# Optimization experiments

Hardware: AMD Instinct MI355X
Metric: run time of the kernel (lower is better)

The kernel has to match this reference:

```python
import jax, jax.numpy as jnp
import numpy as np

# module config (matches init_kwargs, single stream, groups=1)
N, I = 4, 64            # batch, input channels
CR, CA, CO = 64, 64, 64 # recurrent, attention, out channels
HEADS, S = 4, 3         # heads, spatial kernel
HC = CA // HEADS        # head channels = 16
H, W = 48, 48
INIT_I, INIT_F = -1.0, 1.0


def _conv(x, w, padding):
    # x: [N,C,H,W], w: [O,C,kh,kw]
    return jax.lax.conv_general_dilated(
        x, w, window_strides=(1, 1), padding=padding,
        dimension_numbers=('NCHW', 'OIHW', 'NCHW'))


def setup_inputs() -> dict:
    key = jax.random.key(0)
    ks = jax.random.split(key, 8)
    std = 0.05
    x = jax.random.normal(ks[0], (N, I, H, W), jnp.float32)
    W_in = jax.random.normal(ks[1], (CR, I), jnp.float32) * std      # 1x1 input conv
    b_in = jnp.zeros((CR,), jnp.float32)
    # 4 combos (xx, xh, hx, hh), each a 3x3 conv CR->CA, no bias
    Wq = jax.random.normal(ks[2], (4, CA, CR, S, S), jnp.float32) * std * (HC ** -0.5)
    Wk = jax.random.normal(ks[3], (4, CA, CR, S, S), jnp.float32) * std
    Wv = jax.random.normal(ks[4], (4, CA, CR, S, S), jnp.float32) * std
    # gate projections: 4 gates (i,f,g,o) x 4 attn branches, each 1x1 CA->CR
    Wproj = jax.random.normal(ks[5], (4, 4, CR, CA), jnp.float32) * std * 0.5
    b_gates = jnp.array([INIT_I, INIT_F, 0.0, 0.0], jnp.float32)[:, None] * jnp.ones((4, CR), jnp.float32)
    W_out = jax.random.normal(ks[6], (CO, CR), jnp.float32) * std    # 1x1 out conv
    b_out = jnp.zeros((CO,), jnp.float32)
    return {"x": x, "W_in": W_in, "b_in": b_in, "Wq": Wq, "Wk": Wk, "Wv": Wv,
            "Wproj": Wproj, "b_gates": b_gates, "W_out": W_out, "b_out": b_out}


def reference(x, W_in, b_in, Wq, Wk, Wv, Wproj, b_gates, W_out, b_out):
    n, _, hh, ww = x.shape
    # input projection (Accumulate of one 1x1 conv, bias 0)
    xin = jnp.einsum('nchw,oc->nohw', x, W_in) + b_in[None, :, None, None]
    h = jnp.zeros_like(xin)  # cold start: past is empty -> h = c = 0
    pairs = ((xin, xin), (xin, h), (h, xin), (h, h))
    attns = []
    for idx, (query, token) in enumerate(pairs):
        # q: SAME-padded 3x3 conv -> Q = H*W tokens; k/v: VALID -> D = (H-2)*(W-2)
        q = _conv(query, Wq[idx], 'SAME').reshape(n, HEADS, HC, -1)    # [n,h,c,Q]
        k = _conv(token, Wk[idx], 'VALID').reshape(n, HEADS, HC, -1)   # [n,h,c,D]
        v = _conv(token, Wv[idx], 'VALID').reshape(n, HEADS, HC, -1)   # [n,h,c,D]
        w = jax.nn.softmax(jnp.einsum('nhcq,nhcd->nhqd', q, k), axis=-1)
        a = jnp.einsum('nhcd,nhqd->nhcq', v, w).reshape(n, CA, hh, ww)
        attns.append(a)
    A = jnp.stack(attns, axis=0)  # [4, n, CA, H, W]
    # Accumulate of 4 1x1 projections per gate + gate bias
    pre = jnp.einsum('anchw,gaoc->gnohw', A, Wproj) + b_gates[:, None, :, None, None]
    i = jax.nn.sigmoid(pre[0])
    f = jax.nn.sigmoid(pre[1])
    g = jnp.tanh(pre[2])
    o = jax.nn.sigmoid(pre[3])
    c = i * g          # c_prev = 0, so f*c_prev vanishes
    hout = o * jnp.tanh(c)  # dropout p=0 -> identity
    return jnp.einsum('nchw,oc->nohw', hout, W_out) + b_out[None, :, None, None]
```

## Files before the change

### kernel.cpp

```cpp
#include <hip/hip_runtime.h>
#include <math.h>

#define NB   4
#define CIN  64
#define HH   48
#define WW   48
#define HW   2304
#define DH   46
#define DW   46
#define DD   2116
#define NHEAD 4
#define HC   16
#define NT   136
#define QTL  144
#define GS   20000

typedef short  s4 __attribute__((ext_vector_type(4)));
typedef short  s8 __attribute__((ext_vector_type(8)));
typedef float  f4 __attribute__((ext_vector_type(4)));

__device__ __forceinline__ void split4(f4 a, s4& hi, s4& lo) {
    #pragma unroll
    for (int r = 0; r < 4; ++r) {
        unsigned u = __builtin_bit_cast(unsigned, a[r]);
        hi[r] = (short)(u >> 16);
        float l = a[r] - __builtin_bit_cast(float, u & 0xffff0000u);
        lo[r] = (short)(__builtin_bit_cast(unsigned, l) >> 16);
    }
}

__global__ __launch_bounds__(256) void k_xw(const float* __restrict__ x,
                                            const float* __restrict__ Win,
                                            const float* __restrict__ bin,
                                            const float* __restrict__ Wq,
                                            const float* __restrict__ Wk,
                                            const float* __restrict__ Wv,
                                            unsigned short* __restrict__ xb,
                                            unsigned short* __restrict__ Wb,
                                            float* __restrict__ a2m) {
    int b = blockIdx.x;
    if (b == 784) {
        a2m[threadIdx.x] = 0.f;
        return;
    }
    if (b < 640) {
        int bx = b % 10, n = (b / 10) & 3, ocg = b / 40;
        int cell = bx * 256 + threadIdx.x;
        if (cell >= 2500) return;
        int cy = cell / 50, cx = cell - cy * 50;
        float a[4] = {0.f, 0.f, 0.f, 0.f};
        if (cy >= 1 && cy <= 48 && cx >= 1 && cx <= 48) {
            int px = (cy - 1) * 48 + (cx - 1);
            const float* xp = x + (size_t)(n * CIN) * HW + px;
            #pragma unroll
            for (int j = 0; j < 4; ++j) a[j] = bin[ocg * 4 + j];
            #pragma unroll 8
            for (int ic = 0; ic < CIN; ++ic) {
                float xv = xp[ic * HW];
                a[0] += Win[(ocg * 4 + 0) * CIN + ic] * xv;
                a[1] += Win[(ocg * 4 + 1) * CIN + ic] * xv;
                a[2] += Win[(ocg * 4 + 2) * CIN + ic] * xv;
                a[3] += Win[(ocg * 4 + 3) * CIN + ic] * xv;
            }
        }
        s8 st;
        #pragma unroll
        for (int j = 0; j < 4; ++j) {
            unsigned u = __builtin_bit_cast(unsigned, a[j]);
            st[j] = (short)(u >> 16);
            float lo = a[j] - __builtin_bit_cast(float, u & 0xffff0000u);
            st[4 + j] = (short)(__builtin_bit_cast(unsigned, lo) >> 16);
        }
        *(s8*)(xb + ((size_t)(n * 16 + ocg) * 2500 + cell) * 8) = st;
    } else {
        int bx = b - 640;
        int cq = bx / 9, tap = bx - cq * 9;
        int cv = cq >> 2, ocq = cq & 3;
        const float* src = (cv == 0) ? Wq : (cv == 1) ? Wk : (cv == 2) ? Wv
                                                          : (Wv + 2 * CIN * CIN * 9);
        int t = threadIdx.x;
        int m = t >> 4, kl = t & 15, quad = kl >> 2, j = kl & 3;
        #pragma unroll
        for (int kq = 0; kq < 4; ++kq) {
            float v = src[((size_t)(ocq * 16 + m) * CIN + kq * 16 + kl) * 9 + tap];
            unsigned u = __builtin_bit_cast(unsigned, v);
            float lo = v - __builtin_bit_cast(float, u & 0xffff0000u);
            size_t base = ((size_t)(cq * 9 + tap) * 4 + kq) * 512 + m * 32 + quad * 8 + j;
            Wb[base]     = (unsigned short)(u >> 16);
            Wb[base + 4] = (unsigned short)(__builtin_bit_cast(unsigned, lo) >> 16);
        }
    }
}

__global__ __launch_bounds__(256, 3) void k_conv(const unsigned short* __restrict__ xb,
                                                 const unsigned short* __restrict__ Wb,
                                                 unsigned short* __restrict__ Qb,
                                                 float* __restrict__ k0,
                                                 float* __restrict__ v0,
                                                 float* __restrict__ a2m) {
    int y = blockIdx.x, n = blockIdx.y, cv = blockIdx.z;
    int outw = (cv == 0) ? 48 : 46;
    int pd   = (cv == 0) ? 0 : 1;
    if (y >= outw) return;
    int lane = threadIdx.x & 63, wv = threadIdx.x >> 6;
    int m16 = lane & 15, quad = lane >> 4;
    const unsigned short* Wt = Wb + (size_t)(cv * 4 + wv) * 9 * 2048 + m16 * 32 + quad * 8;
    const unsigned short* B0 = xb + (size_t)(n * 16 + quad) * GS
                                  + ((size_t)(y + pd) * 50 + pd + m16) * 8;

    f4 a0 = {0.f, 0.f, 0.f, 0.f}, a1 = a0, a2 = a0;

    s8 w[4], c0[4], c1[4], c2[4];
    #pragma unroll
    for (int kq = 0; kq < 4; ++kq) {
        w[kq]  = *(const s8*)(Wt + kq * 512);
        c0[kq] = *(const s8*)(B0 + (size_t)kq * 4 * GS);
        c1[kq] = *(const s8*)(B0 + (size_t)kq * 4 * GS + 128);
        c2[kq] = *(const s8*)(B0 + (size_t)kq * 4 * GS + 256);
    }
    __builtin_amdgcn_sched_group_barrier(0x020, 16, 0);

    #pragma unroll
    for (int tap = 0; tap < 9; ++tap) {
        s8 wn[4], n0[4], n1[4], n2[4];
        if (tap < 8) {
            int tn = tap + 1;
            int dy = tn / 3, dx = tn - dy * 3;
            const unsigned short* bq = B0 + (size_t)(dy * 50 + dx) * 8;
            const unsigned short* wp = Wt + tn * 2048;
            #pragma unroll
            for (int kq = 0; kq < 4; ++kq) {
                wn[kq] = *(const s8*)(wp + kq * 512);
                n0[kq] = *(const s8*)(bq + (size_t)kq * 4 * GS);
                n1[kq] = *(const s8*)(bq + (size_t)kq * 4 * GS + 128);
                n2[kq] = *(const s8*)(bq + (size_t)kq * 4 * GS + 256);
            }
        }
        #pragma unroll
        for (int kq = 0; kq < 4; ++kq) {
            s4 ah  = __builtin_shufflevector(w[kq], w[kq], 0, 1, 2, 3);
            s4 al  = __builtin_shufflevector(w[kq], w[kq], 4, 5, 6, 7);
            s4 bh0 = __builtin_shufflevector(c0[kq], c0[kq], 0, 1, 2, 3);
            s4 bl0 = __builtin_shufflevector(c0[kq], c0[kq], 4, 5, 6, 7);
            s4 bh1 = __builtin_shufflevector(c1[kq], c1[kq], 0, 1, 2, 3);
            s4 bl1 = __builtin_shufflevector(c1[kq], c1[kq], 4, 5, 6, 7);
            s4 bh2 = __builtin_shufflevector(c2[kq], c2[kq], 0, 1, 2, 3);
            s4 bl2 = __builtin_shufflevector(c2[kq], c2[kq], 4, 5, 6, 7);
            a0 = __builtin_amdgcn_mfma_f32_16x16x16bf16_1k(ah, bh0, a0, 0, 0, 0);
            a1 = __builtin_amdgcn_mfma_f32_16x16x16bf16_1k(ah, bh1, a1, 0, 0, 0);
            a2 = __builtin_amdgcn_mfma_f32_16x16x16bf16_1k(ah, bh2, a2, 0, 0, 0);
            a0 = __builtin_amdgcn_mfma_f32_16x16x16bf16_1k(al, bh0, a0, 0, 0, 0);
            a1 = __builtin_amdgcn_mfma_f32_16x16x16bf16_1k(al, bh1, a1, 0, 0, 0);
            a2 = __builtin_amdgcn_mfma_f32_16x16x16bf16_1k(al, bh2, a2, 0, 0, 0);
            a0 = __builtin_amdgcn_mfma_f32_16x16x16bf16_1k(ah, bl0, a0, 0, 0, 0);
            a1 = __builtin_amdgcn_mfma_f32_16x16x16bf16_1k(ah, bl1, a1, 0, 0, 0);
            a2 = __builtin_amdgcn_mfma_f32_16x16x16bf16_1k(ah, bl2, a2, 0, 0, 0);
        }
        if (tap < 8) __builtin_amdgcn_sched_group_barrier(0x020, 16, 0);
        __builtin_amdgcn_sched_group_barrier(0x008, 36, 0);
        if (tap < 8) {
            #pragma unroll
            for (int kq = 0; kq < 4; ++kq) {
                w[kq] = wn[kq]; c0[kq] = n0[kq]; c1[kq] = n1[kq]; c2[kq] = n2[kq];
            }
        }
    }

    if (cv == 0) {
        int nh = n * 4 + wv;
        unsigned short* dst = Qb + ((size_t)(nh * QTL + y * 3)) * 512 + m16 * 16 + quad * 4;
        f4 accs[3] = {a0, a1, a2};
        #pragma unroll
        for (int xt = 0; xt < 3; ++xt) {
            s4 hi, lo;
            split4(accs[xt], hi, lo);
            *(s4*)(dst + xt * 512) = hi;
            *(s4*)(dst + xt * 512 + 256) = lo;
        }
    } else if (cv == 3) {
        #pragma unroll
        for (int r = 0; r < 4; ++r) {
            float t = a0[r] + a1[r] + ((m16 < 14) ? a2[r] : 0.f);
            t += __shfl_xor(t, 1); t += __shfl_xor(t, 2);
            t += __shfl_xor(t, 4); t += __shfl_xor(t, 8);
            if (m16 == 0)
                atomicAdd(&a2m[n * CIN + wv * 16 + quad * 4 + r], t);
        }
    } else {
        float* ob = (cv == 1) ? k0 : v0;
        size_t outsz = (size_t)DD;
        float* opb = ob + (size_t)(n * CIN + wv * 16 + quad * 4) * outsz + (size_t)y * DW;
        {
            float* op = opb + m16;
            op[0] = a0.x; op[outsz] = a0.y; op[2 * outsz] = a0.z; op[3 * outsz] = a0.w;
            op = opb + 16 + m16;
            op[0] = a1.x; op[outsz] = a1.y; op[2 * outsz] = a1.z; op[3 * outsz] = a1.w;
        }
        if (32 + m16 < DW) {
            float* op = opb + 32 + m16;
            op[0] = a2.x; op[outsz] = a2.y; op[2 * outsz] = a2.z; op[3 * outsz] = a2.w;
        }
    }
}

__global__ __launch_bounds__(256) void k_cvt(const float* __restrict__ k0,
                                             const float* __restrict__ v0,
                                             unsigned short* __restrict__ Kb,
                                             unsigned short* __restrict__ Vb) {
    __shared__ float sm[272];
    int bx = blockIdx.x, nh = blockIdx.y;
    int n = nh >> 2, h = nh & 3;
    int t = threadIdx.x;
    int c = t >> 4, d = t & 15;
    int dgl = bx * 16 + d;
    float kv = (dgl < DD) ? k0[(size_t)(n * CIN + h * HC + c) * DD + dgl] : 0.f;
    sm[c * 17 + d] = kv;
    __syncthreads();
    {
        int d2 = t >> 4, c2 = t & 15;
        float v = sm[c2 * 17 + d2];
        unsigned u = __builtin_bit_cast(unsigned, v);
        unsigned short* dst = Kb + (size_t)(nh * NT + bx) * 512;
        dst[t] = (unsigned short)(u >> 16);
        float lo = v - __builtin_bit_cast(float, u & 0xffff0000u);
        dst[256 + t] = (unsigned short)(__builtin_bit_cast(unsigned, lo) >> 16);
    }
    {
        float vv = (dgl < DD) ? v0[(size_t)(n * CIN + h * HC + c) * DD + dgl] : 0.f;
        unsigned u = __builtin_bit_cast(unsigned, vv);
        unsigned short* dst = Vb + (size_t)(nh * NT + bx) * 512;
        dst[t] = (unsigned short)(u >> 16);
        float lo = vv - __builtin_bit_cast(float, u & 0xffff0000u);
        dst[256 + t] = (unsigned short)(__builtin_bit_cast(unsigned, lo) >> 16);
    }
}

__global__ __launch_bounds__(256) void k_mattn(const unsigned short* __restrict__ Qb,
                                               const unsigned short* __restrict__ Kb,
                                               const unsigned short* __restrict__ Vb,
                                               float* __restrict__ part) {
    __shared__ float sO[4][4][256];
    __shared__ float sl[4][4][64];
    int strip = blockIdx.x >> 1, hb = blockIdx.x & 1, nh = blockIdx.y;
    int lane = threadIdx.x & 63, wv = threadIdx.x >> 6;
    int ds = hb * 4 + wv;
    int q16 = lane & 15, quad = lane >> 4;
    int foff = q16 * 16 + quad * 4;

    s4 qh[4], ql[4];
    #pragma unroll
    for (int j = 0; j < 4; ++j) {
        const unsigned short* Qp = Qb + (size_t)(nh * QTL + strip * 4 + j) * 512 + foff;
        qh[j] = *(const s4*)(Qp);
        ql[j] = *(const s4*)(Qp + 256);
    }
    f4 O[4];
    float l[4];
    #pragma unroll
    for (int j = 0; j < 4; ++j) { O[j] = (f4){0.f, 0.f, 0.f, 0.f}; l[j] = 0.f; }

    const unsigned short* Kp = Kb + (size_t)(nh * NT + ds * 17) * 512 + foff;
    const unsigned short* Vp = Vb + (size_t)(nh * NT + ds * 17) * 512 + foff;
    s4 khi = *(const s4*)(Kp);
    s4 klo = *(const s4*)(Kp + 256);
    s4 vhi = *(const s4*)(Vp);
    s4 vlo = *(const s4*)(Vp + 256);

    for (int it = 0; it < 17; ++it) {
        int nxt = (it < 16) ? (it + 1) * 512 : 0;
        s4 nkhi = *(const s4*)(Kp + nxt);
        s4 nklo = *(const s4*)(Kp + nxt + 256);
        s4 nvhi = *(const s4*)(Vp + nxt);
        s4 nvlo = *(const s4*)(Vp + nxt + 256);

        #pragma unroll
        for (int j = 0; j < 4; ++j) {
            f4 c1 = (f4){0.f, 0.f, 0.f, 0.f};
            c1 = __builtin_amdgcn_mfma_f32_16x16x16bf16_1k(khi, qh[j], c1, 0, 0, 0);
            c1 = __builtin_amdgcn_mfma_f32_16x16x16bf16_1k(klo, qh[j], c1, 0, 0, 0);
            c1 = __builtin_amdgcn_mfma_f32_16x16x16bf16_1k(khi, ql[j], c1, 0, 0, 0);
            float p0 = __expf(c1.x), p1 = __expf(c1.y);
            float p2 = __expf(c1.z), p3 = __expf(c1.w);
            l[j] += (p0 + p1) + (p2 + p3);
            unsigned u0 = __builtin_bit_cast(unsigned, p0);
            unsigned u1 = __builtin_bit_cast(unsigned, p1);
            unsigned u2 = __builtin_bit_cast(unsigned, p2);
            unsigned u3 = __builtin_bit_cast(unsigned, p3);
            s4 ph;
            ph.x = (short)(u0 >> 16); ph.y = (short)(u1 >> 16);
            ph.z = (short)(u2 >> 16); ph.w = (short)(u3 >> 16);
            float r0 = p0 - __builtin_bit_cast(float, u0 & 0xffff0000u);
            float r1 = p1 - __builtin_bit_cast(float, u1 & 0xffff0000u);
            float r2 = p2 - __builtin_bit_cast(float, u2 & 0xffff0000u);
            float r3 = p3 - __builtin_bit_cast(float, u3 & 0xffff0000u);
            s4 pl;
            pl.x = (short)(__builtin_bit_cast(unsigned, r0) >> 16);
            pl.y = (short)(__builtin_bit_cast(unsigned, r1) >> 16);
            pl.z = (short)(__builtin_bit_cast(unsigned, r2) >> 16);
            pl.w = (short)(__builtin_bit_cast(unsigned, r3) >> 16);
            O[j] = __builtin_amdgcn_mfma_f32_16x16x16bf16_1k(vhi, ph, O[j], 0, 0, 0);
            O[j] = __builtin_amdgcn_mfma_f32_16x16x16bf16_1k(vlo, ph, O[j], 0, 0, 0);
            O[j] = __builtin_amdgcn_mfma_f32_16x16x16bf16_1k(vhi, pl, O[j], 0, 0, 0);
        }
        khi = nkhi; klo = nklo; vhi = nvhi; vlo = nvlo;
    }

    #pragma unroll
    for (int j = 0; j < 4; ++j) {
        sO[wv][j][(quad * 4 + 0) * 16 + q16] = O[j].x;
        sO[wv][j][(quad * 4 + 1) * 16 + q16] = O[j].y;
        sO[wv][j][(quad * 4 + 2) * 16 + q16] = O[j].z;
        sO[wv][j][(quad * 4 + 3) * 16 + q16] = O[j].w;
        sl[wv][j][quad * 16 + q16] = l[j];
    }
    __syncthreads();
    int t = threadIdx.x;
    float* pb = part + (size_t)((nh * 36 + strip) * 2 + hb) * 1280;
    #pragma unroll
    for (int j = 0; j < 4; ++j)
        pb[j * 256 + t] = (sO[0][j][t] + sO[1][j][t]) + (sO[2][j][t] + sO[3][j][t]);
    {
        int j2 = t >> 6, i2 = t & 63;
        pb[1024 + t] = (sl[0][j2][i2] + sl[1][j2][i2]) + (sl[2][j2][i2] + sl[3][j2][i2]);
    }
}

__global__ __launch_bounds__(256) void k_gates(const float* __restrict__ part,
                                               const float* __restrict__ a2m,
                                               const float* __restrict__ Wproj,
                                               const float* __restrict__ bg,
                                               const float* __restrict__ Wout,
                                               const float* __restrict__ bout,
                                               float* __restrict__ out) {
    __shared__ float a0s[64][16];
    __shared__ float wps[3][64][64];
    __shared__ float hs[16][68];
    __shared__ float invs[4][16];
    __shared__ float c2s[3][64];
    int n = blockIdx.y;
    int pt = blockIdx.x;
    int strip = pt >> 2, jq = pt & 3;
    int p0 = pt * 16;
    int tid = threadIdx.x;

    if (tid < 64) {
        int h = tid >> 4, q = tid & 15;
        const float* b0 = part + (size_t)(((n * 4 + h) * 36 + strip) * 2) * 1280;
        const float* b1 = b0 + 1280;
        float s = 0.f;
        #pragma unroll
        for (int quad = 0; quad < 4; ++quad)
            s += b0[1024 + jq * 64 + quad * 16 + q] + b1[1024 + jq * 64 + quad * 16 + q];
        invs[h][q] = 1.f / (s - 60.f);
    } else {
        int gi = (tid - 64) >> 6, o = tid & 63;
        int g = (gi == 0) ? 0 : (gi == 1) ? 2 : 3;
        float acc = bg[g * CIN + o];
        const float* wp = Wproj + ((size_t)(g * 4 + 2) * CIN + o) * CIN;
        const float* am = a2m + n * CIN;
        #pragma unroll 8
        for (int c = 0; c < CIN; ++c) acc += wp[c] * (am[c] * (1.f / 2116.f));
        c2s[gi][o] = acc;
    }
    __syncthreads();

    for (int idx = tid; idx < 1024; idx += 256) {
        int c = idx >> 4, px = idx & 15;
        int h = c >> 4, c16 = c & 15;
        const float* b0 = part + (size_t)(((n * 4 + h) * 36 + strip) * 2) * 1280;
        const float* b1 = b0 + 1280;
        int off = jq * 256 + c16 * 16 + px;
        a0s[c][px] = (b0[off] + b1[off]) * invs[h][px];
    }
    for (int idx = tid; idx < 12288; idx += 256) {
        int o = idx & 63; int rest = idx >> 6; int c = rest & 63; int gi = rest >> 6;
        int g = (gi == 0) ? 0 : (gi == 1) ? 2 : 3;
        wps[gi][c][o] = Wproj[((size_t)(g * 4 + 0) * CIN + o) * CIN + c];
    }
    __syncthreads();

    int o = tid & 63, pg = tid >> 6;
    float pi[4], pgt[4], po[4];
    {
        float ci = c2s[0][o], cg = c2s[1][o], co = c2s[2][o];
        #pragma unroll
        for (int j = 0; j < 4; ++j) { pi[j] = ci; pgt[j] = cg; po[j] = co; }
    }
    const float4* a4 = (const float4*)&a0s[0][0];
    #pragma unroll 4
    for (int c = 0; c < 64; ++c) {
        float4 av = a4[c * 4 + pg];
        float w0 = wps[0][c][o], w1 = wps[1][c][o], w2 = wps[2][c][o];
        pi[0]  += w0 * av.x; pi[1]  += w0 * av.y; pi[2]  += w0 * av.z; pi[3]  += w0 * av.w;
        pgt[0] += w1 * av.x; pgt[1] += w1 * av.y; pgt[2] += w1 * av.z; pgt[3] += w1 * av.w;
        po[0]  += w2 * av.x; po[1]  += w2 * av.y; po[2]  += w2 * av.z; po[3]  += w2 * av.w;
    }
    #pragma unroll
    for (int j = 0; j < 4; ++j) {
        float ii = 1.f / (1.f + __expf(-pi[j]));
        float gg = tanhf(pgt[j]);
        float oo = 1.f / (1.f + __expf(-po[j]));
        float cc = ii * gg;
        hs[pg * 4 + j][o] = oo * tanhf(cc);
    }
    __syncthreads();
    float acc[4];
    float bo = bout[o];
    #pragma unroll
    for (int j = 0; j < 4; ++j) acc[j] = bo;
    const float* wo = Wout + o * CIN;
    #pragma unroll 2
    for (int cg_ = 0; cg_ < 16; ++cg_) {
        float w0 = wo[cg_ * 4 + 0], w1 = wo[cg_ * 4 + 1], w2 = wo[cg_ * 4 + 2], w3 = wo[cg_ * 4 + 3];
        #pragma unroll
        for (int j = 0; j < 4; ++j) {
            const float4 hv = *(const float4*)&hs[pg * 4 + j][cg_ * 4];
            acc[j] += w0 * hv.x + w1 * hv.y + w2 * hv.z + w3 * hv.w;
        }
    }
    #pragma unroll
    for (int j = 0; j < 4; ++j)
        out[(size_t)(n * CIN + o) * HW + p0 + pg * 4 + j] = acc[j];
}

extern "C" void kernel_launch(void* const* d_in, const int* in_sizes, int n_in,
                              void* d_out, int out_size, void* d_ws, size_t ws_size,
                              hipStream_t stream) {
    const float* x     = (const float*)d_in[0];
    const float* W_in  = (const float*)d_in[1];
    const float* b_in  = (const float*)d_in[2];
    const float* Wq    = (const float*)d_in[3];
    const float* Wk    = (const float*)d_in[4];
    const float* Wv    = (const float*)d_in[5];
    const float* Wproj = (const float*)d_in[6];
    const float* b_g   = (const float*)d_in[7];
    const float* W_out = (const float*)d_in[8];
    const float* b_out = (const float*)d_in[9];
    float* out = (float*)d_out;

    float* k0   = (float*)d_ws;
    float* v0   = k0 + 541696;
    float* a2m  = v0 + 541696;
    float* part = a2m + 256;
    unsigned short* Qb = (unsigned short*)(part + 1474560);
    unsigned short* Kb = Qb + (size_t)16 * QTL * 512;
    unsigned short* Vb = Kb + (size_t)16 * NT * 512;
    unsigned short* xb = Vb + (size_t)16 * NT * 512;
    unsigned short* Wb = xb + (size_t)4 * 16 * 2500 * 8;

    k_xw    <<<dim3(785), 256, 0, stream>>>(x, W_in, b_in, Wq, Wk, Wv, xb, Wb, a2m);
    k_conv  <<<dim3(48, 4, 4), 256, 0, stream>>>(xb, Wb, Qb, k0, v0, a2m);
    k_cvt   <<<dim3(136, 16), 256, 0, stream>>>(k0, v0, Kb, Vb);
    k_mattn <<<dim3(72, 16), 256, 0, stream>>>(Qb, Kb, Vb, part);
    k_gates <<<dim3(144, 4), 256, 0, stream>>>(part, a2m, Wproj, b_g, W_out, b_out, out);
}
```

Baseline: 176.4 us.

## Use 16x16x32 bf16 MFMA, write K/V directly from conv, drop convert kernel

```diff
diff --git a/kernel.cpp b/kernel.cpp
--- a/kernel.cpp
+++ b/kernel.cpp
@@ -6,18 +6,22 @@
 #define HH   48
 #define WW   48
 #define HW   2304
-#define DH   46
-#define DW   46
 #define DD   2116
 #define NHEAD 4
 #define HC   16
-#define NT   136
+#define NT   144
 #define QTL  144
-#define GS   20000
+#define PS   40000
 
 typedef short  s4 __attribute__((ext_vector_type(4)));
 typedef short  s8 __attribute__((ext_vector_type(8)));
 typedef float  f4 __attribute__((ext_vector_type(4)));
+typedef __bf16 b8 __attribute__((ext_vector_type(8)));
+
+__device__ __forceinline__ f4 mm32(s8 a, s8 b, f4 c) {
+    return __builtin_amdgcn_mfma_f32_16x16x32_bf16(
+        __builtin_bit_cast(b8, a), __builtin_bit_cast(b8, b), c, 0, 0, 0);
+}
 
 __device__ __forceinline__ void split4(f4 a, s4& hi, s4& lo) {
     #pragma unroll
@@ -37,10 +41,21 @@
                                             const float* __restrict__ Wv,
                                             unsigned short* __restrict__ xb,
                                             unsigned short* __restrict__ Wb,
-                                            float* __restrict__ a2m) {
+                                            float* __restrict__ a2m,
+                                            unsigned short* __restrict__ Kb,
+                                            unsigned short* __restrict__ Vb) {
     int b = blockIdx.x;
     if (b == 784) {
         a2m[threadIdx.x] = 0.f;
+        return;
+    }
+    if (b > 784) {
+        int nh = b - 785;
+        s8 z = (s8){0, 0, 0, 0, 0, 0, 0, 0};
+        for (int i = threadIdx.x; i < 1152; i += 256) {
+            if (i < 384) *(s8*)(Kb + ((size_t)nh * NT + 138) * 512  + (size_t)i * 8) = z;
+            else         *(s8*)(Vb + ((size_t)nh * NT + 138) * 1024 + (size_t)(i - 384) * 8) = z;
+        }
         return;
     }
     if (b < 640) {
@@ -63,15 +78,18 @@
                 a[3] += Win[(ocg * 4 + 3) * CIN + ic] * xv;
             }
         }
-        s8 st;
+        s4 hi, lo;
         #pragma unroll
         for (int j = 0; j < 4; ++j) {
             unsigned u = __builtin_bit_cast(unsigned, a[j]);
-            st[j] = (short)(u >> 16);
-            float lo = a[j] - __builtin_bit_cast(float, u & 0xffff0000u);
-            st[4 + j] = (short)(__builtin_bit_cast(unsigned, lo) >> 16);
-        }
-        *(s8*)(xb + ((size_t)(n * 16 + ocg) * 2500 + cell) * 8) = st;
+            hi[j] = (short)(u >> 16);
+            float l = a[j] - __builtin_bit_cast(float, u & 0xffff0000u);
+            lo[j] = (short)(__builtin_bit_cast(unsigned, l) >> 16);
+        }
+        int p = ocg >> 3, h = (ocg >> 2) & 1, q = ocg & 3;
+        unsigned short* d = xb + ((size_t)(n * 8 + p * 4 + q) * 2500 + cell) * 16 + h * 4;
+        *(s4*)(d)     = hi;
+        *(s4*)(d + 8) = lo;
     } else {
         int bx = b - 640;
         int cq = bx / 9, tap = bx - cq * 9;
@@ -79,15 +97,16 @@
         const float* src = (cv == 0) ? Wq : (cv == 1) ? Wk : (cv == 2) ? Wv
                                                           : (Wv + 2 * CIN * CIN * 9);
         int t = threadIdx.x;
-        int m = t >> 4, kl = t & 15, quad = kl >> 2, j = kl & 3;
+        int m = t >> 4, kl = t & 15, q = kl >> 2, j = kl & 3;
         #pragma unroll
         for (int kq = 0; kq < 4; ++kq) {
+            int p = kq >> 1, h = kq & 1;
             float v = src[((size_t)(ocq * 16 + m) * CIN + kq * 16 + kl) * 9 + tap];
             unsigned u = __builtin_bit_cast(unsigned, v);
             float lo = v - __builtin_bit_cast(float, u & 0xffff0000u);
-            size_t base = ((size_t)(cq * 9 + tap) * 4 + kq) * 512 + m * 32 + quad * 8 + j;
-            Wb[base]     = (unsigned short)(u >> 16);
-            Wb[base + 4] = (unsigned short)(__builtin_bit_cast(unsigned, lo) >> 16);
+            size_t base = ((size_t)(cq * 9 + tap) * 2 + p) * 1024 + (m * 4 + q) * 8 + h * 4 + j;
+            Wb[base]       = (unsigned short)(u >> 16);
+            Wb[base + 512] = (unsigned short)(__builtin_bit_cast(unsigned, lo) >> 16);
         }
     }
 }
@@ -95,81 +114,83 @@
 __global__ __launch_bounds__(256, 3) void k_conv(const unsigned short* __restrict__ xb,
                                                  const unsigned short* __restrict__ Wb,
                                                  unsigned short* __restrict__ Qb,
-                                                 float* __restrict__ k0,
-                                                 float* __restrict__ v0,
+                                                 unsigned short* __restrict__ Kb,
+                                                 unsigned short* __restrict__ Vb,
                                                  float* __restrict__ a2m) {
+    __shared__ float sv[4][16][49];
     int y = blockIdx.x, n = blockIdx.y, cv = blockIdx.z;
     int outw = (cv == 0) ? 48 : 46;
     int pd   = (cv == 0) ? 0 : 1;
     if (y >= outw) return;
     int lane = threadIdx.x & 63, wv = threadIdx.x >> 6;
     int m16 = lane & 15, quad = lane >> 4;
-    const unsigned short* Wt = Wb + (size_t)(cv * 4 + wv) * 9 * 2048 + m16 * 32 + quad * 8;
-    const unsigned short* B0 = xb + (size_t)(n * 16 + quad) * GS
-                                  + ((size_t)(y + pd) * 50 + pd + m16) * 8;
-
-    f4 a0 = {0.f, 0.f, 0.f, 0.f}, a1 = a0, a2 = a0;
-
-    s8 w[4], c0[4], c1[4], c2[4];
-    #pragma unroll
-    for (int kq = 0; kq < 4; ++kq) {
-        w[kq]  = *(const s8*)(Wt + kq * 512);
-        c0[kq] = *(const s8*)(B0 + (size_t)kq * 4 * GS);
-        c1[kq] = *(const s8*)(B0 + (size_t)kq * 4 * GS + 128);
-        c2[kq] = *(const s8*)(B0 + (size_t)kq * 4 * GS + 256);
+    int cq = cv * 4 + wv;
+    const unsigned short* Wt = Wb + (size_t)cq * 9 * 2048 + (m16 * 4 + quad) * 8;
+    const unsigned short* X0 = xb + ((size_t)(n * 8 + quad) * 2500
+                                     + (size_t)(y + pd) * 50 + pd + m16) * 16;
+
+    f4 a0 = {0.f, 0.f, 0.f, 0.f}, a1 = a0, a2c = a0;
+
+    s8 w[4], xr[12];
+    #pragma unroll
+    for (int p = 0; p < 2; ++p) {
+        w[p * 2]     = *(const s8*)(Wt + p * 1024);
+        w[p * 2 + 1] = *(const s8*)(Wt + p * 1024 + 512);
+        #pragma unroll
+        for (int col = 0; col < 3; ++col) {
+            const unsigned short* bq = X0 + (size_t)p * 160000 + col * 256;
+            xr[p * 6 + col * 2]     = *(const s8*)(bq);
+            xr[p * 6 + col * 2 + 1] = *(const s8*)(bq + 8);
+        }
     }
     __builtin_amdgcn_sched_group_barrier(0x020, 16, 0);
 
     #pragma unroll
     for (int tap = 0; tap < 9; ++tap) {
-        s8 wn[4], n0[4], n1[4], n2[4];
+        s8 wn[4], xn[12];
         if (tap < 8) {
             int tn = tap + 1;
             int dy = tn / 3, dx = tn - dy * 3;
-            const unsigned short* bq = B0 + (size_t)(dy * 50 + dx) * 8;
-            const unsigned short* wp = Wt + tn * 2048;
-            #pragma unroll
-            for (int kq = 0; kq < 4; ++kq) {
-                wn[kq] = *(const s8*)(wp + kq * 512);
-                n0[kq] = *(const s8*)(bq + (size_t)kq * 4 * GS);
-                n1[kq] = *(const s8*)(bq + (size_t)kq * 4 * GS + 128);
-                n2[kq] = *(const s8*)(bq + (size_t)kq * 4 * GS + 256);
+            const unsigned short* wp  = Wt + tn * 2048;
+            const unsigned short* bq0 = X0 + (size_t)(dy * 50 + dx) * 16;
+            #pragma unroll
+            for (int p = 0; p < 2; ++p) {
+                wn[p * 2]     = *(const s8*)(wp + p * 1024);
+                wn[p * 2 + 1] = *(const s8*)(wp + p * 1024 + 512);
+                #pragma unroll
+                for (int col = 0; col < 3; ++col) {
+                    const unsigned short* bq = bq0 + (size_t)p * 160000 + col * 256;
+                    xn[p * 6 + col * 2]     = *(const s8*)(bq);
+                    xn[p * 6 + col * 2 + 1] = *(const s8*)(bq + 8);
+                }
             }
         }
         #pragma unroll
-        for (int kq = 0; kq < 4; ++kq) {
-            s4 ah  = __builtin_shufflevector(w[kq], w[kq], 0, 1, 2, 3);
-            s4 al  = __builtin_shufflevector(w[kq], w[kq], 4, 5, 6, 7);
-            s4 bh0 = __builtin_shufflevector(c0[kq], c0[kq], 0, 1, 2, 3);
-            s4 bl0 = __builtin_shufflevector(c0[kq], c0[kq], 4, 5, 6, 7);
-            s4 bh1 = __builtin_shufflevector(c1[kq], c1[kq], 0, 1, 2, 3);
-            s4 bl1 = __builtin_shufflevector(c1[kq], c1[kq], 4, 5, 6, 7);
-            s4 bh2 = __builtin_shufflevector(c2[kq], c2[kq], 0, 1, 2, 3);
-            s4 bl2 = __builtin_shufflevector(c2[kq], c2[kq], 4, 5, 6, 7);
-            a0 = __builtin_amdgcn_mfma_f32_16x16x16bf16_1k(ah, bh0, a0, 0, 0, 0);
-            a1 = __builtin_amdgcn_mfma_f32_16x16x16bf16_1k(ah, bh1, a1, 0, 0, 0);
-            a2 = __builtin_amdgcn_mfma_f32_16x16x16bf16_1k(ah, bh2, a2, 0, 0, 0);
-            a0 = __builtin_amdgcn_mfma_f32_16x16x16bf16_1k(al, bh0, a0, 0, 0, 0);
-            a1 = __builtin_amdgcn_mfma_f32_16x16x16bf16_1k(al, bh1, a1, 0, 0, 0);
-            a2 = __builtin_amdgcn_mfma_f32_16x16x16bf16_1k(al, bh2, a2, 0, 0, 0);
-            a0 = __builtin_amdgcn_mfma_f32_16x16x16bf16_1k(ah, bl0, a0, 0, 0, 0);
-            a1 = __builtin_amdgcn_mfma_f32_16x16x16bf16_1k(ah, bl1, a1, 0, 0, 0);
-            a2 = __builtin_amdgcn_mfma_f32_16x16x16bf16_1k(ah, bl2, a2, 0, 0, 0);
+        for (int p = 0; p < 2; ++p) {
+            a0  = mm32(w[p * 2],     xr[p * 6 + 0], a0);
+            a0  = mm32(w[p * 2 + 1], xr[p * 6 + 0], a0);
+            a0  = mm32(w[p * 2],     xr[p * 6 + 1], a0);
+            a1  = mm32(w[p * 2],     xr[p * 6 + 2], a1);
+            a1  = mm32(w[p * 2 + 1], xr[p * 6 + 2], a1);
+            a1  = mm32(w[p * 2],     xr[p * 6 + 3], a1);
+            a2c = mm32(w[p * 2],     xr[p * 6 + 4], a2c);
+            a2c = mm32(w[p * 2 + 1], xr[p * 6 + 4], a2c);
+            a2c = mm32(w[p * 2],     xr[p * 6 + 5], a2c);
         }
         if (tap < 8) __builtin_amdgcn_sched_group_barrier(0x020, 16, 0);
-        __builtin_amdgcn_sched_group_barrier(0x008, 36, 0);
+        __builtin_amdgcn_sched_group_barrier(0x008, 18, 0);
         if (tap < 8) {
             #pragma unroll
-            for (int kq = 0; kq < 4; ++kq) {
-                w[kq] = wn[kq]; c0[kq] = n0[kq]; c1[kq] = n1[kq]; c2[kq] = n2[kq];
-            }
-        }
-    }
-
+            for (int i = 0; i < 4; ++i)  w[i]  = wn[i];
+            #pragma unroll
+            for (int i = 0; i < 12; ++i) xr[i] = xn[i];
+        }
+    }
+
+    f4 accs[3] = {a0, a1, a2c};
+    int nh = n * 4 + wv;
     if (cv == 0) {
-        int nh = n * 4 + wv;
         unsigned short* dst = Qb + ((size_t)(nh * QTL + y * 3)) * 512 + m16 * 16 + quad * 4;
-        f4 accs[3] = {a0, a1, a2};
         #pragma unroll
         for (int xt = 0; xt < 3; ++xt) {
             s4 hi, lo;
@@ -180,58 +201,47 @@
     } else if (cv == 3) {
         #pragma unroll
         for (int r = 0; r < 4; ++r) {
-            float t = a0[r] + a1[r] + ((m16 < 14) ? a2[r] : 0.f);
+            float t = a0[r] + a1[r] + ((m16 < 14) ? a2c[r] : 0.f);
             t += __shfl_xor(t, 1); t += __shfl_xor(t, 2);
             t += __shfl_xor(t, 4); t += __shfl_xor(t, 8);
             if (m16 == 0)
                 atomicAdd(&a2m[n * CIN + wv * 16 + quad * 4 + r], t);
         }
+    } else if (cv == 1) {
+        unsigned short* dst = Kb + ((size_t)nh * NT + y * 3) * 512 + (m16 * 4 + quad) * 8;
+        s8 z = (s8){0, 0, 0, 0, 0, 0, 0, 0};
+        #pragma unroll
+        for (int xt = 0; xt < 3; ++xt) {
+            s4 hi, lo;
+            split4(accs[xt], hi, lo);
+            s8 st = __builtin_shufflevector(hi, lo, 0, 1, 2, 3, 4, 5, 6, 7);
+            if (xt == 2 && m16 >= 14) st = z;
+            *(s8*)(dst + xt * 512) = st;
+        }
     } else {
-        float* ob = (cv == 1) ? k0 : v0;
-        size_t outsz = (size_t)DD;
-        float* opb = ob + (size_t)(n * CIN + wv * 16 + quad * 4) * outsz + (size_t)y * DW;
-        {
-            float* op = opb + m16;
-            op[0] = a0.x; op[outsz] = a0.y; op[2 * outsz] = a0.z; op[3 * outsz] = a0.w;
-            op = opb + 16 + m16;
-            op[0] = a1.x; op[outsz] = a1.y; op[2 * outsz] = a1.z; op[3 * outsz] = a1.w;
-        }
-        if (32 + m16 < DW) {
-            float* op = opb + 32 + m16;
-            op[0] = a2.x; op[outsz] = a2.y; op[2 * outsz] = a2.z; op[3 * outsz] = a2.w;
-        }
-    }
-}
-
-__global__ __launch_bounds__(256) void k_cvt(const float* __restrict__ k0,
-                                             const float* __restrict__ v0,
-                                             unsigned short* __restrict__ Kb,
-                                             unsigned short* __restrict__ Vb) {
-    __shared__ float sm[272];
-    int bx = blockIdx.x, nh = blockIdx.y;
-    int n = nh >> 2, h = nh & 3;
-    int t = threadIdx.x;
-    int c = t >> 4, d = t & 15;
-    int dgl = bx * 16 + d;
-    float kv = (dgl < DD) ? k0[(size_t)(n * CIN + h * HC + c) * DD + dgl] : 0.f;
-    sm[c * 17 + d] = kv;
-    __syncthreads();
-    {
-        int d2 = t >> 4, c2 = t & 15;
-        float v = sm[c2 * 17 + d2];
-        unsigned u = __builtin_bit_cast(unsigned, v);
-        unsigned short* dst = Kb + (size_t)(nh * NT + bx) * 512;
-        dst[t] = (unsigned short)(u >> 16);
-        float lo = v - __builtin_bit_cast(float, u & 0xffff0000u);
-        dst[256 + t] = (unsigned short)(__builtin_bit_cast(unsigned, lo) >> 16);
-    }
-    {
-        float vv = (dgl < DD) ? v0[(size_t)(n * CIN + h * HC + c) * DD + dgl] : 0.f;
-        unsigned u = __builtin_bit_cast(unsigned, vv);
-        unsigned short* dst = Vb + (size_t)(nh * NT + bx) * 512;
-        dst[t] = (unsigned short)(u >> 16);
-        float lo = vv - __builtin_bit_cast(float, u & 0xffff0000u);
-        dst[256 + t] = (unsigned short)(__builtin_bit_cast(unsigned, lo) >> 16);
+        #pragma unroll
+        for (int xt = 0; xt < 3; ++xt)
+            #pragma unroll
+            for (int r = 0; r < 4; ++r)
+                sv[wv][quad * 4 + r][xt * 16 + m16] = accs[xt][r];
+        __syncthreads();
+        int c = lane >> 2, dq = lane & 3;
+        unsigned short* vb = Vb + ((size_t)nh * NT + y * 3) * 1024 + lane * 8;
+        #pragma unroll
+        for (int xt = 0; xt < 3; ++xt) {
+            f4 v;
+            #pragma unroll
+            for (int j = 0; j < 4; ++j) {
+                int xx = xt * 16 + dq * 4 + j;
+                v[j] = (xx < 46) ? sv[wv][c][xx] : 0.f;
+            }
+            s4 hi, lo;
+            split4(v, hi, lo);
+            s8 h2 = __builtin_shufflevector(hi, hi, 0, 1, 2, 3, 0, 1, 2, 3);
+            s8 l2 = __builtin_shufflevector(lo, lo, 0, 1, 2, 3, 0, 1, 2, 3);
+            *(s8*)(vb + xt * 1024)       = h2;
+            *(s8*)(vb + xt * 1024 + 512) = l2;
+        }
     }
 }
 
@@ -245,40 +255,40 @@
     int lane = threadIdx.x & 63, wv = threadIdx.x >> 6;
     int ds = hb * 4 + wv;
     int q16 = lane & 15, quad = lane >> 4;
-    int foff = q16 * 16 + quad * 4;
-
-    s4 qh[4], ql[4];
+
+    s8 qhh[4], qll[4];
     #pragma unroll
     for (int j = 0; j < 4; ++j) {
-        const unsigned short* Qp = Qb + (size_t)(nh * QTL + strip * 4 + j) * 512 + foff;
-        qh[j] = *(const s4*)(Qp);
-        ql[j] = *(const s4*)(Qp + 256);
+        const unsigned short* Qp = Qb + (size_t)(nh * QTL + strip * 4 + j) * 512
+                                     + q16 * 16 + quad * 4;
+        s4 qh = *(const s4*)(Qp);
+        s4 ql = *(const s4*)(Qp + 256);
+        qhh[j] = __builtin_shufflevector(qh, qh, 0, 1, 2, 3, 0, 1, 2, 3);
+        qll[j] = __builtin_shufflevector(ql, ql, 0, 1, 2, 3, 0, 1, 2, 3);
     }
     f4 O[4];
     float l[4];
     #pragma unroll
     for (int j = 0; j < 4; ++j) { O[j] = (f4){0.f, 0.f, 0.f, 0.f}; l[j] = 0.f; }
 
-    const unsigned short* Kp = Kb + (size_t)(nh * NT + ds * 17) * 512 + foff;
-    const unsigned short* Vp = Vb + (size_t)(nh * NT + ds * 17) * 512 + foff;
-    s4 khi = *(const s4*)(Kp);
-    s4 klo = *(const s4*)(Kp + 256);
-    s4 vhi = *(const s4*)(Vp);
-    s4 vlo = *(const s4*)(Vp + 256);
-
-    for (int it = 0; it < 17; ++it) {
-        int nxt = (it < 16) ? (it + 1) * 512 : 0;
-        s4 nkhi = *(const s4*)(Kp + nxt);
-        s4 nklo = *(const s4*)(Kp + nxt + 256);
-        s4 nvhi = *(const s4*)(Vp + nxt);
-        s4 nvlo = *(const s4*)(Vp + nxt + 256);
+    const unsigned short* Kp = Kb + (size_t)(nh * NT + ds * 18) * 512  + (q16 * 4 + quad) * 8;
+    const unsigned short* Vp = Vb + (size_t)(nh * NT + ds * 18) * 1024 + (q16 * 4 + quad) * 8;
+    s8 kk = *(const s8*)(Kp);
+    s8 vh = *(const s8*)(Vp);
+    s8 vl = *(const s8*)(Vp + 512);
+
+    for (int it = 0; it < 18; ++it) {
+        int nk = (it < 17) ? (it + 1) * 512 : 0;
+        int nv = (it < 17) ? (it + 1) * 1024 : 0;
+        s8 nkk = *(const s8*)(Kp + nk);
+        s8 nvh = *(const s8*)(Vp + nv);
+        s8 nvl = *(const s8*)(Vp + nv + 512);
 
         #pragma unroll
         for (int j = 0; j < 4; ++j) {
             f4 c1 = (f4){0.f, 0.f, 0.f, 0.f};
-            c1 = __builtin_amdgcn_mfma_f32_16x16x16bf16_1k(khi, qh[j], c1, 0, 0, 0);
-            c1 = __builtin_amdgcn_mfma_f32_16x16x16bf16_1k(klo, qh[j], c1, 0, 0, 0);
-            c1 = __builtin_amdgcn_mfma_f32_16x16x16bf16_1k(khi, ql[j], c1, 0, 0, 0);
+            c1 = mm32(kk, qhh[j], c1);
+            c1 = mm32(kk, qll[j], c1);
             float p0 = __expf(c1.x), p1 = __expf(c1.y);
             float p2 = __expf(c1.z), p3 = __expf(c1.w);
             l[j] += (p0 + p1) + (p2 + p3);
@@ -286,31 +296,29 @@
             unsigned u1 = __builtin_bit_cast(unsigned, p1);
             unsigned u2 = __builtin_bit_cast(unsigned, p2);
             unsigned u3 = __builtin_bit_cast(unsigned, p3);
-            s4 ph;
-            ph.x = (short)(u0 >> 16); ph.y = (short)(u1 >> 16);
-            ph.z = (short)(u2 >> 16); ph.w = (short)(u3 >> 16);
             float r0 = p0 - __builtin_bit_cast(float, u0 & 0xffff0000u);
             float r1 = p1 - __builtin_bit_cast(float, u1 & 0xffff0000u);
             float r2 = p2 - __builtin_bit_cast(float, u2 & 0xffff0000u);
             float r3 = p3 - __builtin_bit_cast(float, u3 & 0xffff0000u);
-            s4 pl;
-            pl.x = (short)(__builtin_bit_cast(unsigned, r0) >> 16);
-            pl.y = (short)(__builtin_bit_cast(unsigned, r1) >> 16);
-            pl.z = (short)(__builtin_bit_cast(unsigned, r2) >> 16);
-            pl.w = (short)(__builtin_bit_cast(unsigned, r3) >> 16);
-            O[j] = __builtin_amdgcn_mfma_f32_16x16x16bf16_1k(vhi, ph, O[j], 0, 0, 0);
-            O[j] = __builtin_amdgcn_mfma_f32_16x16x16bf16_1k(vlo, ph, O[j], 0, 0, 0);
-            O[j] = __builtin_amdgcn_mfma_f32_16x16x16bf16_1k(vhi, pl, O[j], 0, 0, 0);
-        }
-        khi = nkhi; klo = nklo; vhi = nvhi; vlo = nvlo;
+            s8 pp;
+            pp[0] = (short)(u0 >> 16); pp[1] = (short)(u1 >> 16);
+            pp[2] = (short)(u2 >> 16); pp[3] = (short)(u3 >> 16);
+            pp[4] = (short)(__builtin_bit_cast(unsigned, r0) >> 16);
+            pp[5] = (short)(__builtin_bit_cast(unsigned, r1) >> 16);
+            pp[6] = (short)(__builtin_bit_cast(unsigned, r2) >> 16);
+            pp[7] = (short)(__builtin_bit_cast(unsigned, r3) >> 16);
+            O[j] = mm32(pp, vh, O[j]);
+            O[j] = mm32(pp, vl, O[j]);
+        }
+        kk = nkk; vh = nvh; vl = nvl;
     }
 
     #pragma unroll
     for (int j = 0; j < 4; ++j) {
-        sO[wv][j][(quad * 4 + 0) * 16 + q16] = O[j].x;
-        sO[wv][j][(quad * 4 + 1) * 16 + q16] = O[j].y;
-        sO[wv][j][(quad * 4 + 2) * 16 + q16] = O[j].z;
-        sO[wv][j][(quad * 4 + 3) * 16 + q16] = O[j].w;
+        sO[wv][j][q16 * 16 + quad * 4 + 0] = O[j].x;
+        sO[wv][j][q16 * 16 + quad * 4 + 1] = O[j].y;
+        sO[wv][j][q16 * 16 + quad * 4 + 2] = O[j].z;
+        sO[wv][j][q16 * 16 + quad * 4 + 3] = O[j].w;
         sl[wv][j][quad * 16 + q16] = l[j];
     }
     __syncthreads();
@@ -351,7 +359,7 @@
         #pragma unroll
         for (int quad = 0; quad < 4; ++quad)
             s += b0[1024 + jq * 64 + quad * 16 + q] + b1[1024 + jq * 64 + quad * 16 + q];
-        invs[h][q] = 1.f / (s - 60.f);
+        invs[h][q] = 1.f / (s - 188.f);
     } else {
         int gi = (tid - 64) >> 6, o = tid & 63;
         int g = (gi == 0) ? 0 : (gi == 1) ? 2 : 3;
@@ -438,19 +446,16 @@
     const float* b_out = (const float*)d_in[9];
     float* out = (float*)d_out;
 
-    float* k0   = (float*)d_ws;
-    float* v0   = k0 + 541696;
-    float* a2m  = v0 + 541696;
+    float* a2m  = (float*)d_ws;
     float* part = a2m + 256;
     unsigned short* Qb = (unsigned short*)(part + 1474560);
     unsigned short* Kb = Qb + (size_t)16 * QTL * 512;
     unsigned short* Vb = Kb + (size_t)16 * NT * 512;
-    unsigned short* xb = Vb + (size_t)16 * NT * 512;
-    unsigned short* Wb = xb + (size_t)4 * 16 * 2500 * 8;
-
-    k_xw    <<<dim3(785), 256, 0, stream>>>(x, W_in, b_in, Wq, Wk, Wv, xb, Wb, a2m);
-    k_conv  <<<dim3(48, 4, 4), 256, 0, stream>>>(xb, Wb, Qb, k0, v0, a2m);
-    k_cvt   <<<dim3(136, 16), 256, 0, stream>>>(k0, v0, Kb, Vb);
+    unsigned short* xb = Vb + (size_t)16 * NT * 1024;
+    unsigned short* Wb = xb + (size_t)32 * 2500 * 16;
+
+    k_xw    <<<dim3(801), 256, 0, stream>>>(x, W_in, b_in, Wq, Wk, Wv, xb, Wb, a2m, Kb, Vb);
+    k_conv  <<<dim3(48, 4, 4), 256, 0, stream>>>(xb, Wb, Qb, Kb, Vb, a2m);
     k_mattn <<<dim3(72, 16), 256, 0, stream>>>(Qb, Kb, Vb, part);
     k_gates <<<dim3(144, 4), 256, 0, stream>>>(part, a2m, Wproj, b_g, W_out, b_out, out);
 }
```

Result: no change. 175.3 us (median of 2 runs) (-0.6%).
